# Performance work log

Hardware: AMD Instinct MI355X
Metric: run time of the kernel (lower is better)

## Reference

```python
import jax, jax.numpy as jnp
import numpy as np

EPS = 1e-5
NEG_SLOPE = 0.01  # torch F.leaky_relu default


def _batchnorm(h, gamma, beta):
    # BatchNorm1d in training mode: batch stats over node dim, biased variance
    mu = jnp.mean(h, axis=0)
    var = jnp.mean((h - mu) ** 2, axis=0)
    return gamma * (h - mu) * jax.lax.rsqrt(var + EPS) + beta


def setup_inputs() -> dict:
    N, E, H, ED = 16384, 524288, 128, 16
    key = jax.random.key(0)
    ks = jax.random.split(key, 12)
    s = 1.0 / np.sqrt(H)
    return {
        "x": jax.random.normal(ks[0], (N, H), jnp.float32),
        "edge_index": jax.random.randint(ks[1], (2, E), 0, N, jnp.int64),
        "edge_attr": jax.random.normal(ks[2], (E, ED), jnp.float32),
        "Wq": jax.random.normal(ks[3], (H, H), jnp.float32) * s,
        "bq": jnp.zeros((H,), jnp.float32),
        "Wk": jax.random.normal(ks[4], (H, H), jnp.float32) * s,
        "bk": jnp.zeros((H,), jnp.float32),
        "Wv": jax.random.normal(ks[5], (H, H), jnp.float32) * s,
        "bv": jnp.zeros((H,), jnp.float32),
        "We": jax.random.normal(ks[6], (ED, 1), jnp.float32) * (1.0 / np.sqrt(ED)),
        "be": jnp.zeros((1,), jnp.float32),
        "bn1_g": jnp.ones((H,), jnp.float32),
        "bn1_b": jnp.zeros((H,), jnp.float32),
        "W1": jax.random.normal(ks[7], (H, 2 * H), jnp.float32) * s,
        "b1": jnp.zeros((2 * H,), jnp.float32),
        "W2": jax.random.normal(ks[8], (2 * H, H), jnp.float32) * (1.0 / np.sqrt(2 * H)),
        "b2": jnp.zeros((H,), jnp.float32),
        "bn2_g": jnp.ones((H,), jnp.float32),
        "bn2_b": jnp.zeros((H,), jnp.float32),
    }


def reference(x, edge_index, edge_attr, Wq, bq, Wk, bk, Wv, bv, We, be,
              bn1_g, bn1_b, W1, b1, W2, b2, bn2_g, bn2_b):
    N = x.shape[0]
    Q = x @ Wq + bq  # [N, H]
    K = x @ Wk + bk
    V = x @ Wv + bv
    Ebias = (edge_attr @ We + be)[:, 0]  # [E], num_heads == 1
    src, dst = edge_index[0], edge_index[1]
    # per-edge dot product over the FULL hidden dim (as in the source)
    scores = jnp.sum(Q[src] * K[dst], axis=1) + Ebias  # [E]
    scores = jnp.where(scores >= 0, scores, NEG_SLOPE * scores)
    # to_dense_adj scatter-adds edge_attr into a dense [N, N] adjacency
    adj = jnp.zeros((N, N), x.dtype).at[src, dst].add(scores)
    attn = jax.nn.softmax(adj, axis=1)  # dense softmax incl. zero non-edges
    x_new = attn @ V  # [N, H]
    h = _batchnorm(x + x_new, bn1_g, bn1_b)
    ffn = jax.nn.relu(h @ W1 + b1) @ W2 + b2
    return _batchnorm(h + ffn, bn2_g, bn2_b)
```

## Files before the change

### kernel.cpp

```cpp
#include <hip/hip_runtime.h>
#include <hip/hip_bf16.h>
#include <math.h>

#define H 128
#define H2 256
#define SLAB 96
#define LDA 136
#define LDA2 264
#define EPS 1e-5f

typedef __attribute__((ext_vector_type(8))) short s16x8;
typedef __attribute__((ext_vector_type(4))) float f32x4;

__device__ __forceinline__ unsigned short f2bf(float f) {
  unsigned u = __float_as_uint(f);
  unsigned r = (u + 0x7FFFu + ((u >> 16) & 1u)) >> 16;
  return (unsigned short)r;
}
__device__ __forceinline__ float bf2f(unsigned short s) {
  return __uint_as_float(((unsigned)s) << 16);
}
__device__ __forceinline__ unsigned short f2h(float f) {
  union { unsigned short s; _Float16 h; } c; c.h = (_Float16)f; return c.s;
}
__device__ __forceinline__ float h2f(unsigned short u) {
  union { unsigned short s; _Float16 h; } c; c.s = u; return (float)c.h;
}

__global__ void wprep(const float* __restrict__ Wq, const float* __restrict__ Wk,
                      const float* __restrict__ Wv, const float* __restrict__ W1,
                      const float* __restrict__ W2,
                      short* qh, short* kh, short* vh, short* w1h, short* w2h,
                      int* __restrict__ cnt, float* __restrict__ stats, int N)
{
  int job = blockIdx.z;
  if (job == 5) {
    int t = blockIdx.x * 256 + threadIdx.x;
    if (t < N) cnt[t] = 0;
    for (int s = t; s < 264 * H; s += 32768) stats[s] = 0.f;
    return;
  }
  const float* src; short* dh; int Kd, Nn; bool ashalf;
  if (job == 0)      { src = Wq; dh = qh;  Kd = 128; Nn = 128; ashalf = true; }
  else if (job == 1) { src = Wk; dh = kh;  Kd = 128; Nn = 128; ashalf = true; }
  else if (job == 2) { src = Wv; dh = vh;  Kd = 128; Nn = 128; ashalf = true; }
  else if (job == 3) { src = W1; dh = w1h; Kd = 128; Nn = 256; ashalf = false; }
  else               { src = W2; dh = w2h; Kd = 256; Nn = 128; ashalf = false; }
  int t = blockIdx.x * 256 + threadIdx.x;
  if (t >= Kd * Nn) return;
  int n = t / Kd, k = t - n * Kd;
  float v = src[(size_t)k * Nn + n];
  dh[t] = ashalf ? (short)f2h(v) : (short)f2bf(v);
}

__global__ __launch_bounds__(256) void qkv_mfma(
    const float* __restrict__ x,
    const short* __restrict__ Wqh, const short* __restrict__ Wkh,
    const short* __restrict__ Wvh,
    const float* __restrict__ bq, const float* __restrict__ bk,
    const float* __restrict__ bv,
    unsigned short* __restrict__ Qh, unsigned short* __restrict__ Kh,
    unsigned short* __restrict__ Vh, float* __restrict__ SVp,
    const float* __restrict__ ea, const float* __restrict__ We,
    const float* __restrict__ be, float* __restrict__ Eb,
    int E, int nqkv)
{
  __shared__ __align__(16) short A[64 * LDA];
  int tid = threadIdx.x;

  if (blockIdx.x >= nqkv) {
    int e = (blockIdx.x - nqkv) * 256 + tid;
    if (e < E) {
      float4 w0 = *(const float4*)&We[0], w1 = *(const float4*)&We[4];
      float4 w2 = *(const float4*)&We[8], w3 = *(const float4*)&We[12];
      const float4* p = (const float4*)&ea[(size_t)e * 16];
      float4 a0 = p[0], a1 = p[1], a2 = p[2], a3 = p[3];
      float s = a0.x * w0.x + a0.y * w0.y + a0.z * w0.z + a0.w * w0.w
              + a1.x * w1.x + a1.y * w1.y + a1.z * w1.z + a1.w * w1.w
              + a2.x * w2.x + a2.y * w2.y + a2.z * w2.z + a2.w * w2.w
              + a3.x * w3.x + a3.y * w3.y + a3.z * w3.z + a3.w * w3.w;
      Eb[e] = s + be[0];
    }
    return;
  }

  int bm = blockIdx.x * 64;
  int wave = tid >> 6, lane = tid & 63;
  int quad = lane >> 4, l16 = lane & 15;
  int wn = wave * 32;

#pragma unroll
  for (int i = 0; i < 4; ++i) {
    int g = i * 256 + tid;
    int row = g >> 4, f = g & 15;
    const float4* xp = (const float4*)&x[(size_t)(bm + row) * H + f * 8];
    float4 v0 = xp[0], v1 = xp[1];
    float vv[8] = {v0.x, v0.y, v0.z, v0.w, v1.x, v1.y, v1.z, v1.w};
    s16x8 hv;
#pragma unroll
    for (int j = 0; j < 8; ++j) hv[j] = (short)f2h(vv[j]);
    *(s16x8*)&A[row * LDA + f * 8] = hv;
  }
  __syncthreads();

  for (int ph = 0; ph < 3; ++ph) {
    const short* Bh = (ph == 0) ? Wqh : (ph == 1) ? Wkh : Wvh;

    s16x8 bh[2][4];
#pragma unroll
    for (int nt = 0; nt < 2; ++nt)
#pragma unroll
      for (int ks = 0; ks < 4; ++ks)
        bh[nt][ks] = *(const s16x8*)&Bh[(size_t)(wn + nt * 16 + l16) * H + ks * 32 + quad * 8];

    f32x4 acc[4][2];
#pragma unroll
    for (int mt = 0; mt < 4; ++mt)
#pragma unroll
      for (int nt = 0; nt < 2; ++nt) acc[mt][nt] = (f32x4){0.f, 0.f, 0.f, 0.f};

#pragma unroll
    for (int ks = 0; ks < 4; ++ks) {
      int kof = ks * 32 + quad * 8;
      s16x8 ah[4];
#pragma unroll
      for (int mt = 0; mt < 4; ++mt)
        ah[mt] = *(s16x8*)&A[(mt * 16 + l16) * LDA + kof];
#pragma unroll
      for (int mt = 0; mt < 4; ++mt)
#pragma unroll
        for (int nt = 0; nt < 2; ++nt)
          acc[mt][nt] = __builtin_amdgcn_mfma_f32_16x16x32_f16(ah[mt], bh[nt][ks], acc[mt][nt], 0, 0, 0);
    }

    if (ph == 0) {
#pragma unroll
      for (int nt = 0; nt < 2; ++nt) {
        int col = wn + nt * 16 + l16;
        float bb = bq[col];
#pragma unroll
        for (int mt = 0; mt < 4; ++mt)
#pragma unroll
          for (int r = 0; r < 4; ++r) {
            int row = bm + mt * 16 + quad * 4 + r;
            Qh[(size_t)row * H + col] = f2h(acc[mt][nt][r] + bb);
          }
      }
    } else if (ph == 1) {
#pragma unroll
      for (int nt = 0; nt < 2; ++nt) {
        int col = wn + nt * 16 + l16;
        float bb = bk[col];
#pragma unroll
        for (int mt = 0; mt < 4; ++mt)
#pragma unroll
          for (int r = 0; r < 4; ++r) {
            int row = bm + mt * 16 + quad * 4 + r;
            Kh[(size_t)row * H + col] = f2h(acc[mt][nt][r] + bb);
          }
      }
    } else {
      int bank = blockIdx.x & 7;
#pragma unroll
      for (int nt = 0; nt < 2; ++nt) {
        int col = wn + nt * 16 + l16;
        float bb = bv[col];
        float ps = 0.f;
#pragma unroll
        for (int mt = 0; mt < 4; ++mt)
#pragma unroll
          for (int r = 0; r < 4; ++r) {
            int row = bm + mt * 16 + quad * 4 + r;
            float v = acc[mt][nt][r] + bb;
            Vh[(size_t)row * H + col] = f2h(v);
            ps += v;
          }
        ps += __shfl_xor(ps, 16);
        ps += __shfl_xor(ps, 32);
        if (quad == 0) atomicAdd(&SVp[bank * H + col], ps);
      }
    }
  }
}

__global__ __launch_bounds__(256) void ebfill(
    const int* __restrict__ ei,
    const float* __restrict__ Eb,
    const unsigned short* __restrict__ Qh,
    const unsigned short* __restrict__ Kh,
    int* __restrict__ cnt,
    int2* __restrict__ slabDE, int E, int N)
{
  __shared__ int qeP[2048];
  __shared__ float qeB[2048];
  __shared__ int qn;
  int tid = threadIdx.x;
  int grp = blockIdx.x & 7;
  int blk = blockIdx.x >> 3;
  int lo = grp * (N >> 3), hi = lo + (N >> 3);
  int per = E >> 8;
  int base = blk * per;
  const int* eiD = ei + E;

  if (tid == 0) qn = 0;
  __syncthreads();

  for (int i = 0; i < per; i += 256) {
    int e = base + i + tid;
    if (e >= E) continue;
    int src = ei[e];
    int dst = eiD[e];
    float b = Eb[e];
    if (src >= lo && src < hi) {
      int p = atomicAdd(&qn, 1);
      qeP[p] = (dst << 11) | (src - lo);
      qeB[p] = b;
    }
  }
  __syncthreads();

  int m = qn;
  int sub = tid & 7, st = tid >> 3;
  int j = st;
  for (; j + 32 < m; j += 64) {
    int pA = qeP[j], pB = qeP[j + 32];
    float bA = qeB[j], bB = qeB[j + 32];
    int sA = lo + (pA & 2047), dA = pA >> 11;
    int sB = lo + (pB & 2047), dB = pB >> 11;
    const s16x8* qpA = (const s16x8*)(Qh + (size_t)sA * H);
    const s16x8* kpA = (const s16x8*)(Kh + (size_t)dA * H);
    const s16x8* qpB = (const s16x8*)(Qh + (size_t)sB * H);
    const s16x8* kpB = (const s16x8*)(Kh + (size_t)dB * H);
    s16x8 qa0 = qpA[sub], qb0 = qpA[8 + sub];
    s16x8 ka0 = kpA[sub], kb0 = kpA[8 + sub];
    s16x8 qa1 = qpB[sub], qb1 = qpB[8 + sub];
    s16x8 ka1 = kpB[sub], kb1 = kpB[8 + sub];
    float s0 = 0.f, s1 = 0.f;
#pragma unroll
    for (int u = 0; u < 8; ++u) {
      s0 += h2f((unsigned short)qa0[u]) * h2f((unsigned short)ka0[u]);
      s0 += h2f((unsigned short)qb0[u]) * h2f((unsigned short)kb0[u]);
      s1 += h2f((unsigned short)qa1[u]) * h2f((unsigned short)ka1[u]);
      s1 += h2f((unsigned short)qb1[u]) * h2f((unsigned short)kb1[u]);
    }
    s0 += __shfl_xor(s0, 1); s1 += __shfl_xor(s1, 1);
    s0 += __shfl_xor(s0, 2); s1 += __shfl_xor(s1, 2);
    s0 += __shfl_xor(s0, 4); s1 += __shfl_xor(s1, 4);
    if (sub == 0) {
      s0 += bA; s1 += bB;
      s0 = (s0 >= 0.f) ? s0 : 0.01f * s0;
      s1 = (s1 >= 0.f) ? s1 : 0.01f * s1;
      int posA = atomicAdd(&cnt[sA], 1);
      if (posA < SLAB) {
        int2 rec; rec.x = dA; rec.y = __float_as_int(s0);
        slabDE[sA * SLAB + posA] = rec;
      }
      int posB = atomicAdd(&cnt[sB], 1);
      if (posB < SLAB) {
        int2 rec; rec.x = dB; rec.y = __float_as_int(s1);
        slabDE[sB * SLAB + posB] = rec;
      }
    }
  }
  for (; j < m; j += 32) {
    int p = qeP[j];
    float b = qeB[j];
    int src = lo + (p & 2047), dst = p >> 11;
    const s16x8* qp = (const s16x8*)(Qh + (size_t)src * H);
    const s16x8* kp = (const s16x8*)(Kh + (size_t)dst * H);
    s16x8 qa = qp[sub], qb = qp[8 + sub];
    s16x8 ka = kp[sub], kb = kp[8 + sub];
    float s = 0.f;
#pragma unroll
    for (int u = 0; u < 8; ++u) {
      s += h2f((unsigned short)qa[u]) * h2f((unsigned short)ka[u]);
      s += h2f((unsigned short)qb[u]) * h2f((unsigned short)kb[u]);
    }
    s += __shfl_xor(s, 1);
    s += __shfl_xor(s, 2);
    s += __shfl_xor(s, 4);
    if (sub == 0) {
      s += b;
      s = (s >= 0.f) ? s : 0.01f * s;
      int pos = atomicAdd(&cnt[src], 1);
      if (pos < SLAB) {
        int2 rec; rec.x = dst; rec.y = __float_as_int(s);
        slabDE[src * SLAB + pos] = rec;
      }
    }
  }
}

__global__ __launch_bounds__(256) void attn_fused(
    const float* __restrict__ x,
    const unsigned short* __restrict__ Vh,
    const float* __restrict__ SVp, const int* __restrict__ cnt,
    const int2* __restrict__ slabDE,
    float* __restrict__ h1, float* __restrict__ sum1p, float* __restrict__ sq1p,
    int N)
{
  __shared__ float sv[4][SLAB];
  __shared__ int sd[4][SLAB];
  __shared__ short sown[4][SLAB];
  __shared__ float csum[H], csq[H];
  int tid = threadIdx.x;
  int team = tid >> 6, lane = tid & 63;
  int grp = blockIdx.x & 7;
  int r = blockIdx.x >> 3;
  int i = grp * (N >> 3) + r * 4 + team;
  int k = cnt[i]; if (k > SLAB) k = SLAB;
  int base = i * SLAB;

  if (tid < H) { csum[tid] = 0.f; csq[tid] = 0.f; }
  __syncthreads();

  for (int p = lane; p < k; p += 64) {
    int2 de = slabDE[base + p];
    sd[team][p] = de.x;
    sv[team][p] = __int_as_float(de.y);
  }

  float2 xx = *(const float2*)&x[(size_t)i * H + lane * 2];
  float sx = 0.f, sy = 0.f;
#pragma unroll
  for (int b = 0; b < 8; ++b) {
    float2 t = *(const float2*)&SVp[b * H + lane * 2];
    sx += t.x; sy += t.y;
  }

  for (int p = lane; p < k; p += 64) {
    int d = sd[team][p];
    int o = p;
    for (int q = p - 1; q >= 0; --q)
      o = (sd[team][q] == d) ? q : o;
    sown[team][p] = (short)o;
  }
  for (int p = lane; p < k; p += 64) {
    int o = sown[team][p];
    if (o != p) atomicAdd(&sv[team][o], sv[team][p]);
  }

  float mx = 0.f;
  for (int p = lane; p < k; p += 64)
    if (sown[team][p] == (short)p) mx = fmaxf(mx, sv[team][p]);
#pragma unroll
  for (int msk = 32; msk; msk >>= 1) mx = fmaxf(mx, __shfl_xor(mx, msk));
  float em = __expf(-mx);

  float zl = 0.f;
  for (int p = lane; p < k; p += 64) {
    float cf = 0.f;
    if (sown[team][p] == (short)p) cf = __expf(sv[team][p] - mx) - em;
    sv[team][p] = cf;
    zl += cf;
  }
#pragma unroll
  for (int msk = 32; msk; msk >>= 1) zl += __shfl_xor(zl, msk);
  float Zi = 1.f / ((float)N * em + zl);

  const ushort2* V2 = (const ushort2*)Vh;
  float ax = em * sx, ay = em * sy;
  int c = 0;
  for (; c + 8 <= k; c += 8) {
    float cf[8]; int dd[8]; ushort2 vv[8];
#pragma unroll
    for (int u = 0; u < 8; ++u) { cf[u] = sv[team][c + u]; dd[u] = sd[team][c + u]; }
#pragma unroll
    for (int u = 0; u < 8; ++u) vv[u] = V2[(size_t)dd[u] * 64 + lane];
#pragma unroll
    for (int u = 0; u < 8; ++u) {
      ax += cf[u] * h2f(vv[u].x);
      ay += cf[u] * h2f(vv[u].y);
    }
  }
  for (; c < k; ++c) {
    float cf = sv[team][c];
    ushort2 v0 = V2[(size_t)sd[team][c] * 64 + lane];
    ax += cf * h2f(v0.x); ay += cf * h2f(v0.y);
  }
  float ox = xx.x + ax * Zi;
  float oy = xx.y + ay * Zi;
  float2 ov; ov.x = ox; ov.y = oy;
  *(float2*)&h1[(size_t)i * H + lane * 2] = ov;

  int c0 = lane * 2;
  atomicAdd(&csum[c0 + 0], ox); atomicAdd(&csq[c0 + 0], ox * ox);
  atomicAdd(&csum[c0 + 1], oy); atomicAdd(&csq[c0 + 1], oy * oy);
  __syncthreads();
  if (tid < H) {
    int bank = blockIdx.x & 63;
    atomicAdd(&sum1p[bank * H + tid], csum[tid]);
    atomicAdd(&sq1p[bank * H + tid], csq[tid]);
  }
}

__global__ __launch_bounds__(256) void ffn_fused(
    const float* __restrict__ h1, const short* __restrict__ W1h,
    const float* __restrict__ b1, const short* __restrict__ W2h,
    const float* __restrict__ b2,
    const float* __restrict__ sum1p, const float* __restrict__ sq1p,
    const float* __restrict__ g1, const float* __restrict__ bb1,
    float* __restrict__ h2, float* __restrict__ sum2p, float* __restrict__ sq2p,
    float invN)
{
  __shared__ __align__(16) short As[32 * LDA];
  __shared__ __align__(16) short Ts[32 * LDA2];
  __shared__ float aF[H], bF[H];
  int tid = threadIdx.x;
  int bm = blockIdx.x * 32;
  int wave = tid >> 6, lane = tid & 63;
  int quad = lane >> 4, l16 = lane & 15;

  if (tid < H) {
    float s = 0.f, q = 0.f;
#pragma unroll
    for (int b = 0; b < 64; ++b) { s += sum1p[b * H + tid]; q += sq1p[b * H + tid]; }
    float mu = s * invN;
    float var = q * invN - mu * mu;
    float rs = rsqrtf(var + EPS);
    float a = g1[tid] * rs;
    aF[tid] = a;
    bF[tid] = bb1[tid] - a * mu;
  }
  __syncthreads();

  int f = tid & 15;
#pragma unroll
  for (int i = 0; i < 2; ++i) {
    int g = i * 256 + tid;
    int row = g >> 4;
    const float4* xp = (const float4*)&h1[(size_t)(bm + row) * H + f * 8];
    float4 v0 = xp[0], v1 = xp[1];
    float vv[8] = {v0.x, v0.y, v0.z, v0.w, v1.x, v1.y, v1.z, v1.w};
    s16x8 hv;
#pragma unroll
    for (int j = 0; j < 8; ++j) {
      int c = f * 8 + j;
      hv[j] = (short)f2bf(aF[c] * vv[j] + bF[c]);
    }
    *(s16x8*)&As[row * LDA + f * 8] = hv;
  }

  int wn1 = wave * 64;
  s16x8 b1f[4][4];
#pragma unroll
  for (int nt = 0; nt < 4; ++nt)
#pragma unroll
    for (int ks = 0; ks < 4; ++ks)
      b1f[nt][ks] = *(const s16x8*)&W1h[(size_t)(wn1 + nt * 16 + l16) * H + ks * 32 + quad * 8];
  __syncthreads();

  f32x4 acc1[2][4];
#pragma unroll
  for (int mt = 0; mt < 2; ++mt)
#pragma unroll
    for (int nt = 0; nt < 4; ++nt) acc1[mt][nt] = (f32x4){0.f, 0.f, 0.f, 0.f};

#pragma unroll
  for (int ks = 0; ks < 4; ++ks) {
    int kof = ks * 32 + quad * 8;
    s16x8 ah[2];
#pragma unroll
    for (int mt = 0; mt < 2; ++mt) ah[mt] = *(s16x8*)&As[(mt * 16 + l16) * LDA + kof];
#pragma unroll
    for (int mt = 0; mt < 2; ++mt)
#pragma unroll
      for (int nt = 0; nt < 4; ++nt)
        acc1[mt][nt] = __builtin_amdgcn_mfma_f32_16x16x32_bf16(ah[mt], b1f[nt][ks], acc1[mt][nt], 0, 0, 0);
  }

#pragma unroll
  for (int nt = 0; nt < 4; ++nt) {
    int col = wn1 + nt * 16 + l16;
    float bb = b1[col];
#pragma unroll
    for (int mt = 0; mt < 2; ++mt)
#pragma unroll
      for (int r = 0; r < 4; ++r) {
        int row = mt * 16 + quad * 4 + r;
        float v = acc1[mt][nt][r] + bb;
        v = v > 0.f ? v : 0.f;
        Ts[row * LDA2 + col] = (short)f2bf(v);
      }
  }

  int wn2 = wave * 32;
  s16x8 b2f[2][8];
#pragma unroll
  for (int nt = 0; nt < 2; ++nt)
#pragma unroll
    for (int ks = 0; ks < 8; ++ks)
      b2f[nt][ks] = *(const s16x8*)&W2h[(size_t)(wn2 + nt * 16 + l16) * H2 + ks * 32 + quad * 8];
  __syncthreads();

  f32x4 acc2[2][2];
#pragma unroll
  for (int mt = 0; mt < 2; ++mt)
#pragma unroll
    for (int nt = 0; nt < 2; ++nt) acc2[mt][nt] = (f32x4){0.f, 0.f, 0.f, 0.f};

#pragma unroll
  for (int ks = 0; ks < 8; ++ks) {
    int kof = ks * 32 + quad * 8;
    s16x8 ah[2];
#pragma unroll
    for (int mt = 0; mt < 2; ++mt) ah[mt] = *(s16x8*)&Ts[(mt * 16 + l16) * LDA2 + kof];
#pragma unroll
    for (int mt = 0; mt < 2; ++mt)
#pragma unroll
      for (int nt = 0; nt < 2; ++nt)
        acc2[mt][nt] = __builtin_amdgcn_mfma_f32_16x16x32_bf16(ah[mt], b2f[nt][ks], acc2[mt][nt], 0, 0, 0);
  }

  int bank = blockIdx.x & 63;
#pragma unroll
  for (int nt = 0; nt < 2; ++nt) {
    int col = wn2 + nt * 16 + l16;
    float ra = aF[col], rb = bF[col];
    float bb = b2[col];
    float ps = 0.f, pq = 0.f;
#pragma unroll
    for (int mt = 0; mt < 2; ++mt)
#pragma unroll
      for (int r = 0; r < 4; ++r) {
        int row = bm + mt * 16 + quad * 4 + r;
        float rr = ra * h1[(size_t)row * H + col] + rb;
        float v = acc2[mt][nt][r] + bb + rr;
        h2[(size_t)row * H + col] = v;
        ps += v; pq += v * v;
      }
    ps += __shfl_xor(ps, 16); ps += __shfl_xor(ps, 32);
    pq += __shfl_xor(pq, 16); pq += __shfl_xor(pq, 32);
    if (quad == 0) {
      atomicAdd(&sum2p[bank * H + col], ps);
      atomicAdd(&sq2p[bank * H + col], pq);
    }
  }
}

__global__ __launch_bounds__(256) void bn_apply(
    const float* __restrict__ X,
    const float* __restrict__ sum2p, const float* __restrict__ sq2p,
    const float* __restrict__ g2, const float* __restrict__ bb2,
    float* __restrict__ Y, size_t n4, float invN)
{
  __shared__ float A2s[H], B2s[H];
  int tid = threadIdx.x;
  if (tid < H) {
    float s = 0.f, q = 0.f;
#pragma unroll
    for (int b = 0; b < 64; ++b) { s += sum2p[b * H + tid]; q += sq2p[b * H + tid]; }
    float mu = s * invN;
    float var = q * invN - mu * mu;
    float rs = rsqrtf(var + EPS);
    float a = g2[tid] * rs;
    A2s[tid] = a;
    B2s[tid] = bb2[tid] - a * mu;
  }
  __syncthreads();
  size_t i = (size_t)blockIdx.x * blockDim.x + tid;
  if (i >= n4) return;
  float4 v = ((const float4*)X)[i];
  int c = (int)((i * 4) & (H - 1));
  float4 a = *(const float4*)&A2s[c];
  float4 b = *(const float4*)&B2s[c];
  v.x = a.x * v.x + b.x; v.y = a.y * v.y + b.y;
  v.z = a.z * v.z + b.z; v.w = a.w * v.w + b.w;
  ((float4*)Y)[i] = v;
}

extern "C" void kernel_launch(void* const* d_in, const int* in_sizes, int n_in,
                              void* d_out, int out_size, void* d_ws, size_t ws_size,
                              hipStream_t stream)
{
  const float* x  = (const float*)d_in[0];
  const int*   ei = (const int*)d_in[1];
  const float* ea = (const float*)d_in[2];
  const float* Wq = (const float*)d_in[3];
  const float* bq = (const float*)d_in[4];
  const float* Wk = (const float*)d_in[5];
  const float* bk = (const float*)d_in[6];
  const float* Wv = (const float*)d_in[7];
  const float* bv = (const float*)d_in[8];
  const float* We = (const float*)d_in[9];
  const float* be = (const float*)d_in[10];
  const float* g1 = (const float*)d_in[11];
  const float* bb1 = (const float*)d_in[12];
  const float* W1 = (const float*)d_in[13];
  const float* b1 = (const float*)d_in[14];
  const float* W2 = (const float*)d_in[15];
  const float* b2 = (const float*)d_in[16];
  const float* g2 = (const float*)d_in[17];
  const float* bb2 = (const float*)d_in[18];

  int N = in_sizes[0] / H;
  int E = in_sizes[2] / 16;
  size_t NH = (size_t)N * H;
  float invN = 1.0f / (float)N;

  unsigned short* Qh = (unsigned short*)d_ws;
  unsigned short* Kh = Qh + NH;
  unsigned short* Vh = Kh + NH;
  float* h1  = (float*)(Vh + NH);
  int2*  slabDE = (int2*)(h1 + NH);
  int*   cnt    = (int*)(slabDE + (size_t)N * SLAB);
  float* stats  = (float*)(cnt + N);
  float* SVp   = stats;
  float* sum1p = stats + 8 * H;
  float* sq1p  = sum1p + 64 * H;
  float* sum2p = sq1p + 64 * H;
  float* sq2p  = sum2p + 64 * H;
  float* statsEnd = sq2p + 64 * H;
  short* wbuf = (short*)statsEnd;
  short* Wqf = wbuf;
  short* Wkf = Wqf + 16384;
  short* Wvf = Wkf + 16384;
  short* W1h = Wvf + 16384;
  short* W2h = W1h + 32768;
  float* Eb  = (float*)(W2h + 32768);
  float* h2 = (float*)Qh;

  int nqkv = N / 64;
  int nebias = (E + 255) / 256;

  wprep<<<dim3(128, 1, 6), 256, 0, stream>>>(Wq, Wk, Wv, W1, W2,
      Wqf, Wkf, Wvf, W1h, W2h, cnt, stats, N);

  qkv_mfma<<<dim3(nqkv + nebias), 256, 0, stream>>>(
      x, Wqf, Wkf, Wvf, bq, bk, bv, Qh, Kh, Vh, SVp,
      ea, We, be, Eb, E, nqkv);

  ebfill<<<dim3(2048), 256, 0, stream>>>(ei, Eb, Qh, Kh, cnt, slabDE, E, N);

  attn_fused<<<dim3(N / 4), 256, 0, stream>>>(x, Vh, SVp, cnt, slabDE,
                                              h1, sum1p, sq1p, N);

  ffn_fused<<<dim3(N / 32), 256, 0, stream>>>(h1, W1h, b1, W2h, b2,
      sum1p, sq1p, g1, bb1, h2, sum2p, sq2p, invN);

  bn_apply<<<dim3((int)((NH / 4 + 255) / 256)), 256, 0, stream>>>(
      h2, sum2p, sq2p, g2, bb2, (float*)d_out, NH / 4, invN);
}
```

Baseline: 223.6 us.

## Pre-bucket edges by source range during edge-bias pass to avoid rescans

The edge-bias blocks in the QKV kernel now also read the edge indices and scatter packed (src,dst,bias) records into 8 global buckets keyed by source range, using shared-memory counters plus one global atomic per bucket per block. ebfill then reads its bucket slice directly instead of having each of 8 groups rescan all edges and filter by source. This removes redundant reads of edge_index and the bias array, at the cost of extra global writes and a fixed bucket capacity that could drop edges if skewed.

```diff
diff --git a/kernel.cpp b/kernel.cpp
--- a/kernel.cpp
+++ b/kernel.cpp
@@ -8,6 +8,7 @@
 #define LDA 136
 #define LDA2 264
 #define EPS 1e-5f
+#define BKCAP 69632
 
 typedef __attribute__((ext_vector_type(8))) short s16x8;
 typedef __attribute__((ext_vector_type(4))) float f32x4;
@@ -37,7 +38,7 @@
   if (job == 5) {
     int t = blockIdx.x * 256 + threadIdx.x;
     if (t < N) cnt[t] = 0;
-    for (int s = t; s < 264 * H; s += 32768) stats[s] = 0.f;
+    for (int s = t; s < 264 * H + 256; s += 32768) stats[s] = 0.f;
     return;
   }
   const float* src; short* dh; int Kd, Nn; bool ashalf;
@@ -62,24 +63,60 @@
     unsigned short* __restrict__ Qh, unsigned short* __restrict__ Kh,
     unsigned short* __restrict__ Vh, float* __restrict__ SVp,
     const float* __restrict__ ea, const float* __restrict__ We,
-    const float* __restrict__ be, float* __restrict__ Eb,
+    const float* __restrict__ be, const int* __restrict__ ei,
+    int* __restrict__ bcnt, int2* __restrict__ bedge,
     int E, int nqkv)
 {
   __shared__ __align__(16) short A[64 * LDA];
+  __shared__ int lcnt[8];
+  __shared__ int lbase[8];
   int tid = threadIdx.x;
 
   if (blockIdx.x >= nqkv) {
-    int e = (blockIdx.x - nqkv) * 256 + tid;
-    if (e < E) {
-      float4 w0 = *(const float4*)&We[0], w1 = *(const float4*)&We[4];
-      float4 w2 = *(const float4*)&We[8], w3 = *(const float4*)&We[12];
-      const float4* p = (const float4*)&ea[(size_t)e * 16];
-      float4 a0 = p[0], a1 = p[1], a2 = p[2], a3 = p[3];
-      float s = a0.x * w0.x + a0.y * w0.y + a0.z * w0.z + a0.w * w0.w
-              + a1.x * w1.x + a1.y * w1.y + a1.z * w1.z + a1.w * w1.w
-              + a2.x * w2.x + a2.y * w2.y + a2.z * w2.z + a2.w * w2.w
-              + a3.x * w3.x + a3.y * w3.y + a3.z * w3.z + a3.w * w3.w;
-      Eb[e] = s + be[0];
+    int blk = blockIdx.x - nqkv;
+    int base = blk * 1024;
+    if (tid < 8) lcnt[tid] = 0;
+    __syncthreads();
+
+    float4 w0 = *(const float4*)&We[0], w1 = *(const float4*)&We[4];
+    float4 w2 = *(const float4*)&We[8], w3 = *(const float4*)&We[12];
+    float bias = be[0];
+
+    int bId[4], lpos[4], px[4]; float sc[4];
+#pragma unroll
+    for (int i = 0; i < 4; ++i) {
+      int e = base + i * 256 + tid;
+      bId[i] = -1;
+      if (e < E) {
+        const float4* p = (const float4*)&ea[(size_t)e * 16];
+        float4 a0 = p[0], a1 = p[1], a2 = p[2], a3 = p[3];
+        float s = a0.x * w0.x + a0.y * w0.y + a0.z * w0.z + a0.w * w0.w
+                + a1.x * w1.x + a1.y * w1.y + a1.z * w1.z + a1.w * w1.w
+                + a2.x * w2.x + a2.y * w2.y + a2.z * w2.z + a2.w * w2.w
+                + a3.x * w3.x + a3.y * w3.y + a3.z * w3.z + a3.w * w3.w;
+        s += bias;
+        int src = ei[e];
+        int dst = ei[E + e];
+        int b = src >> 11;
+        bId[i] = b;
+        px[i] = (src << 14) | dst;
+        sc[i] = s;
+        lpos[i] = atomicAdd(&lcnt[b], 1);
+      }
+    }
+    __syncthreads();
+    if (tid < 8 && lcnt[tid] > 0)
+      lbase[tid] = atomicAdd(&bcnt[tid * 32], lcnt[tid]);
+    __syncthreads();
+#pragma unroll
+    for (int i = 0; i < 4; ++i) {
+      if (bId[i] >= 0) {
+        int pos = lbase[bId[i]] + lpos[i];
+        if (pos < BKCAP) {
+          int2 rec; rec.x = px[i]; rec.y = __float_as_int(sc[i]);
+          bedge[(size_t)bId[i] * BKCAP + pos] = rec;
+        }
+      }
     }
     return;
   }
@@ -184,49 +221,29 @@
 }
 
 __global__ __launch_bounds__(256) void ebfill(
-    const int* __restrict__ ei,
-    const float* __restrict__ Eb,
+    const int2* __restrict__ bedge, const int* __restrict__ bcnt,
     const unsigned short* __restrict__ Qh,
     const unsigned short* __restrict__ Kh,
     int* __restrict__ cnt,
-    int2* __restrict__ slabDE, int E, int N)
+    int2* __restrict__ slabDE, int N)
 {
-  __shared__ int qeP[2048];
-  __shared__ float qeB[2048];
-  __shared__ int qn;
   int tid = threadIdx.x;
   int grp = blockIdx.x & 7;
   int blk = blockIdx.x >> 3;
-  int lo = grp * (N >> 3), hi = lo + (N >> 3);
-  int per = E >> 8;
-  int base = blk * per;
-  const int* eiD = ei + E;
-
-  if (tid == 0) qn = 0;
-  __syncthreads();
-
-  for (int i = 0; i < per; i += 256) {
-    int e = base + i + tid;
-    if (e >= E) continue;
-    int src = ei[e];
-    int dst = eiD[e];
-    float b = Eb[e];
-    if (src >= lo && src < hi) {
-      int p = atomicAdd(&qn, 1);
-      qeP[p] = (dst << 11) | (src - lo);
-      qeB[p] = b;
-    }
-  }
-  __syncthreads();
-
-  int m = qn;
+  int m = bcnt[grp * 32]; if (m > BKCAP) m = BKCAP;
+  const int2* be = bedge + (size_t)grp * BKCAP;
+  int chunk = (m + 255) >> 8;
+  int start = blk * chunk;
+  int end = start + chunk; if (end > m) end = m;
   int sub = tid & 7, st = tid >> 3;
-  int j = st;
-  for (; j + 32 < m; j += 64) {
-    int pA = qeP[j], pB = qeP[j + 32];
-    float bA = qeB[j], bB = qeB[j + 32];
-    int sA = lo + (pA & 2047), dA = pA >> 11;
-    int sB = lo + (pB & 2047), dB = pB >> 11;
+
+  int j = start + st;
+  for (; j + 32 < end; j += 64) {
+    int2 rA = be[j];
+    int2 rB = be[j + 32];
+    int sA = rA.x >> 14, dA = rA.x & 16383;
+    int sB = rB.x >> 14, dB = rB.x & 16383;
+    float bA = __int_as_float(rA.y), bB = __int_as_float(rB.y);
     const s16x8* qpA = (const s16x8*)(Qh + (size_t)sA * H);
     const s16x8* kpA = (const s16x8*)(Kh + (size_t)dA * H);
     const s16x8* qpB = (const s16x8*)(Qh + (size_t)sB * H);
@@ -253,19 +270,19 @@
       int posA = atomicAdd(&cnt[sA], 1);
       if (posA < SLAB) {
         int2 rec; rec.x = dA; rec.y = __float_as_int(s0);
-        slabDE[sA * SLAB + posA] = rec;
+        slabDE[(size_t)sA * SLAB + posA] = rec;
       }
       int posB = atomicAdd(&cnt[sB], 1);
       if (posB < SLAB) {
         int2 rec; rec.x = dB; rec.y = __float_as_int(s1);
-        slabDE[sB * SLAB + posB] = rec;
-      }
-    }
-  }
-  for (; j < m; j += 32) {
-    int p = qeP[j];
-    float b = qeB[j];
-    int src = lo + (p & 2047), dst = p >> 11;
+        slabDE[(size_t)sB * SLAB + posB] = rec;
+      }
+    }
+  }
+  for (; j < end; j += 32) {
+    int2 r = be[j];
+    int src = r.x >> 14, dst = r.x & 16383;
+    float b = __int_as_float(r.y);
     const s16x8* qp = (const s16x8*)(Qh + (size_t)src * H);
     const s16x8* kp = (const s16x8*)(Kh + (size_t)dst * H);
     s16x8 qa = qp[sub], qb = qp[8 + sub];
@@ -285,7 +302,7 @@
       int pos = atomicAdd(&cnt[src], 1);
       if (pos < SLAB) {
         int2 rec; rec.x = dst; rec.y = __float_as_int(s);
-        slabDE[src * SLAB + pos] = rec;
+        slabDE[(size_t)src * SLAB + pos] = rec;
       }
     }
   }
@@ -610,27 +627,27 @@
   float* sq1p  = sum1p + 64 * H;
   float* sum2p = sq1p + 64 * H;
   float* sq2p  = sum2p + 64 * H;
-  float* statsEnd = sq2p + 64 * H;
-  short* wbuf = (short*)statsEnd;
+  int*   bcnt  = (int*)(sq2p + 64 * H);
+  short* wbuf = (short*)(bcnt + 256);
   short* Wqf = wbuf;
   short* Wkf = Wqf + 16384;
   short* Wvf = Wkf + 16384;
   short* W1h = Wvf + 16384;
   short* W2h = W1h + 32768;
-  float* Eb  = (float*)(W2h + 32768);
+  int2*  bedge = (int2*)(W2h + 32768);
   float* h2 = (float*)Qh;
 
   int nqkv = N / 64;
-  int nebias = (E + 255) / 256;
+  int nscat = (E + 1023) / 1024;
 
   wprep<<<dim3(128, 1, 6), 256, 0, stream>>>(Wq, Wk, Wv, W1, W2,
       Wqf, Wkf, Wvf, W1h, W2h, cnt, stats, N);
 
-  qkv_mfma<<<dim3(nqkv + nebias), 256, 0, stream>>>(
+  qkv_mfma<<<dim3(nqkv + nscat), 256, 0, stream>>>(
       x, Wqf, Wkf, Wvf, bq, bk, bv, Qh, Kh, Vh, SVp,
-      ea, We, be, Eb, E, nqkv);
-
-  ebfill<<<dim3(2048), 256, 0, stream>>>(ei, Eb, Qh, Kh, cnt, slabDE, E, N);
+      ea, We, be, ei, bcnt, bedge, E, nqkv);
+
+  ebfill<<<dim3(2048), 256, 0, stream>>>(bedge, bcnt, Qh, Kh, cnt, slabDE, N);
 
   attn_fused<<<dim3(N / 4), 256, 0, stream>>>(x, Vh, SVp, cnt, slabDE,
                                               h1, sum1p, sq1p, N);
```

Measured after the change: 223.8 us. No clear change (+0.1%).
